# Optimization experiments

Hardware: AMD Instinct MI355X
Metric: run time of the kernel (lower is better)

Reference implementation:

```python
import jax, jax.numpy as jnp
import numpy as np

B, D, C = 8192, 64, 2048
BETA = 0.25
EPS = 1e-6


def setup_inputs() -> dict:
    key = jax.random.key(0)
    k1, k2, k3 = jax.random.split(key, 3)
    x = jax.random.normal(k1, (B, D), dtype=jnp.float32)
    prev_q = jax.random.normal(k2, (B, D), dtype=jnp.float32)
    codes = jax.random.normal(k3, (1, C, D), dtype=jnp.float32) * 0.1  # learned codebook param
    return {"x": x, "prev_q": prev_q, "codes": codes}


def _rotation_matrix(u, v, eps=EPS):
    # u: (B, D) unit vectors, v: (D,) unit vector. Rodrigues-like rotation mapping v -> u.
    uvT = u[:, :, None] * v[None, None, :]          # (B, D, D)
    vuT = v[None, :, None] * u[:, None, :]          # (B, D, D)
    A = uvT - vuT
    A2 = jnp.einsum('bij,bjk->bik', A, A)
    dot = jnp.sum(u * v[None, :], axis=-1)[:, None, None]  # (B,1,1)
    I = jnp.eye(u.shape[-1], dtype=u.dtype)
    return I[None] + A + A2 / (1.0 + dot + eps)


def reference(x, prev_q, codes):
    # F.normalize(prev_q, dim=-1, eps=1e-6)
    norm = jnp.linalg.norm(prev_q, axis=-1, keepdims=True)
    u = prev_q / jnp.maximum(norm, EPS)
    v = jnp.full((D,), 1.0 / float(D) ** 0.5, dtype=x.dtype)  # registered buffer v

    R = _rotation_matrix(u, v)                      # (B, D, D); R_inv = R^T
    x_canonical = jnp.einsum('bij,bi->bj', R, x)    # R^T @ x

    c0 = codes[0]                                   # (C, D)
    # squared L2 distances (B, C) via GEMM expansion (same math as sum((x-c)^2))
    dists = (jnp.sum(x_canonical ** 2, axis=-1, keepdims=True)
             - 2.0 * (x_canonical @ c0.T)
             + jnp.sum(c0 ** 2, axis=-1)[None, :])
    indices = jnp.argmin(dists, axis=-1)            # (B,)
    quantized_canonical = c0[indices]               # (B, D)

    # STE: value equals quantized_canonical, gradient flows to x_canonical
    q_out = x_canonical + jax.lax.stop_gradient(quantized_canonical - x_canonical)
    quantized = jnp.einsum('bij,bj->bi', R, q_out)  # R @ q_out

    loss_commit = jnp.mean(jnp.sum((x - jax.lax.stop_gradient(quantized_canonical)) ** 2, axis=-1))
    loss_codebook = jnp.mean(jnp.sum((jax.lax.stop_gradient(x) - quantized_canonical) ** 2, axis=-1))
    loss = loss_commit + BETA * loss_codebook
    return quantized, indices, loss
```

## Files before the change

kernel.cpp:

```cpp
#include <hip/hip_runtime.h>
#include <math.h>

#define B_ROWS 8192
#define DIM 64
#define NCODES 2048
#define NSPLIT 16
#define CODES_PER_SPLIT (NCODES / NSPLIT)
#define TILES_PER_WAVE (CODES_PER_SPLIT / 16)
#define EPSF 1e-6f
#define BETA 0.25f
#define V_VAL 0.125f

typedef __attribute__((ext_vector_type(8))) short sh8;
typedef __attribute__((ext_vector_type(4))) float f32x4;

__device__ __forceinline__ float wave_sum64(float v) {
#pragma unroll
    for (int m = 32; m >= 1; m >>= 1) v += __shfl_xor(v, m, 64);
    return v;
}

__device__ __forceinline__ unsigned short f2bf(float f) {
    unsigned u = __float_as_uint(f);
    unsigned r = (u + 0x7fffu + ((u >> 16) & 1u)) >> 16;
    return (unsigned short)r;
}
__device__ __forceinline__ float bf2f(unsigned short h) {
    return __uint_as_float(((unsigned)h) << 16);
}

__device__ __forceinline__ void write_frag3(unsigned short* frag, int rc,
                                            int dim, float val) {
    unsigned short s0 = f2bf(val);
    float r = val - bf2f(s0);
    unsigned short s1 = f2bf(r);
    r -= bf2f(s1);
    unsigned short s2 = f2bf(r);
    int t = rc >> 4, m = rc & 15;
    int h = dim >> 5, q = (dim >> 3) & 3, j = dim & 7;
    int lanep = q * 16 + m;
    size_t base = ((size_t)(t * 3) * 2 + h) * 512 + (size_t)lanep * 8 + j;
    frag[base] = s0;
    frag[base + 2 * 512] = s1;
    frag[base + 4 * 512] = s2;
}

__global__ __launch_bounds__(256) void rq_prep(
        const float* __restrict__ x,
        const float* __restrict__ pq,
        const float* __restrict__ codes,
        float* __restrict__ cn,
        unsigned short* __restrict__ cfrag,
        unsigned short* __restrict__ xfrag,
        float* __restrict__ uo,
        float* __restrict__ duv,
        float* __restrict__ out_loss) {
    int tid = threadIdx.x;
    int lane = tid & 63;
    int w = tid >> 6;

    if (blockIdx.x < NCODES / 4) {
        int c = blockIdx.x * 4 + w;
        float cv = codes[(size_t)c * DIM + lane];
        float s = wave_sum64(cv * cv);
        if (lane == 0) cn[c] = s;
        write_frag3(cfrag, c, lane, cv);
        if (blockIdx.x == 0 && tid == 0) *out_loss = 0.0f;
    } else {
        int r = (blockIdx.x - NCODES / 4) * 4 + w;
        float xv = x[(size_t)r * DIM + lane];
        float qv = pq[(size_t)r * DIM + lane];
        float n2 = wave_sum64(qv * qv);
        float inv = 1.0f / fmaxf(sqrtf(n2), EPSF);
        float uv = qv * inv;
        float d = V_VAL * wave_sum64(uv);
        float a = wave_sum64(uv * xv);
        float b = V_VAL * wave_sum64(xv);
        float den = 1.0f + d + EPSF;
        float cu = -b + (d * b - a) / den;
        float cv = a - (b - d * a) / den;
        float xcv = xv + uv * cu + V_VAL * cv;
        uo[(size_t)r * DIM + lane] = uv;
        if (lane == 0) duv[r] = d;
        write_frag3(xfrag, r, lane, xcv);
    }
}

__global__ __launch_bounds__(256) void rq_dist_mfma(
        const unsigned short* __restrict__ xfrag,
        const unsigned short* __restrict__ cfrag,
        const float* __restrict__ cn,
        float* __restrict__ pd,
        int* __restrict__ pi) {
    int tid = threadIdx.x;
    int lane = tid & 63;
    int w = tid >> 6;
    int rb = blockIdx.x >> 4;
    int cs = blockIdx.x & (NSPLIT - 1);
    int r0 = rb * 128 + w * 32;
    int rt0 = r0 >> 4;

    const sh8* xf = (const sh8*)xfrag;
    const sh8* cf = (const sh8*)cfrag;

    sh8 afr[2][3][2];
#pragma unroll
    for (int rs = 0; rs < 2; ++rs)
#pragma unroll
        for (int s = 0; s < 3; ++s)
#pragma unroll
            for (int h = 0; h < 2; ++h)
                afr[rs][s][h] = xf[(size_t)(((rt0 + rs) * 3 + s) * 2 + h) * 64 + lane];

    float bv0[4], bv1[4];
    int bi0[4], bi1[4];
#pragma unroll
    for (int i = 0; i < 4; ++i) {
        bv0[i] = INFINITY; bv1[i] = INFINITY;
        bi0[i] = 0x7fffffff; bi1[i] = 0x7fffffff;
    }

    int cbase = cs * CODES_PER_SPLIT;
    for (int t = 0; t < TILES_PER_WAVE; ++t) {
        int c0 = cbase + t * 16;
        int ct = c0 >> 4;
        sh8 bfr[3][2];
#pragma unroll
        for (int s = 0; s < 3; ++s)
#pragma unroll
            for (int h = 0; h < 2; ++h)
                bfr[s][h] = cf[(size_t)((ct * 3 + s) * 2 + h) * 64 + lane];

        f32x4 acc0 = {0.f, 0.f, 0.f, 0.f};
        f32x4 acc1 = {0.f, 0.f, 0.f, 0.f};
#pragma unroll
        for (int h = 0; h < 2; ++h) {
            acc0 = __builtin_amdgcn_mfma_f32_16x16x32_bf16(afr[0][2][h], bfr[0][h], acc0, 0, 0, 0);
            acc0 = __builtin_amdgcn_mfma_f32_16x16x32_bf16(afr[0][1][h], bfr[1][h], acc0, 0, 0, 0);
            acc0 = __builtin_amdgcn_mfma_f32_16x16x32_bf16(afr[0][0][h], bfr[2][h], acc0, 0, 0, 0);
            acc0 = __builtin_amdgcn_mfma_f32_16x16x32_bf16(afr[0][1][h], bfr[0][h], acc0, 0, 0, 0);
            acc0 = __builtin_amdgcn_mfma_f32_16x16x32_bf16(afr[0][0][h], bfr[1][h], acc0, 0, 0, 0);
            acc0 = __builtin_amdgcn_mfma_f32_16x16x32_bf16(afr[0][0][h], bfr[0][h], acc0, 0, 0, 0);

            acc1 = __builtin_amdgcn_mfma_f32_16x16x32_bf16(afr[1][2][h], bfr[0][h], acc1, 0, 0, 0);
            acc1 = __builtin_amdgcn_mfma_f32_16x16x32_bf16(afr[1][1][h], bfr[1][h], acc1, 0, 0, 0);
            acc1 = __builtin_amdgcn_mfma_f32_16x16x32_bf16(afr[1][0][h], bfr[2][h], acc1, 0, 0, 0);
            acc1 = __builtin_amdgcn_mfma_f32_16x16x32_bf16(afr[1][1][h], bfr[0][h], acc1, 0, 0, 0);
            acc1 = __builtin_amdgcn_mfma_f32_16x16x32_bf16(afr[1][0][h], bfr[1][h], acc1, 0, 0, 0);
            acc1 = __builtin_amdgcn_mfma_f32_16x16x32_bf16(afr[1][0][h], bfr[0][h], acc1, 0, 0, 0);
        }

        float cnv = cn[c0 + (lane & 15)];
        int idxv = c0 + (lane & 15);
#pragma unroll
        for (int reg = 0; reg < 4; ++reg) {
            float s0 = fmaf(-2.0f, acc0[reg], cnv);
            if (s0 < bv0[reg]) { bv0[reg] = s0; bi0[reg] = idxv; }
            float s1 = fmaf(-2.0f, acc1[reg], cnv);
            if (s1 < bv1[reg]) { bv1[reg] = s1; bi1[reg] = idxv; }
        }
    }

#pragma unroll
    for (int rs = 0; rs < 2; ++rs) {
#pragma unroll
        for (int reg = 0; reg < 4; ++reg) {
            float v = rs ? bv1[reg] : bv0[reg];
            int ix = rs ? bi1[reg] : bi0[reg];
#pragma unroll
            for (int m = 1; m < 16; m <<= 1) {
                float ov = __shfl_xor(v, m, 64);
                int oi = __shfl_xor(ix, m, 64);
                if (ov < v || (ov == v && oi < ix)) { v = ov; ix = oi; }
            }
            int row = r0 + rs * 16 + (lane >> 4) * 4 + reg;
            if ((lane & 15) == reg) {
                pd[(size_t)row * NSPLIT + cs] = v;
                pi[(size_t)row * NSPLIT + cs] = ix;
            }
        }
    }
}

__global__ __launch_bounds__(512) void rq_epilogue(
        const float* __restrict__ x,
        const float* __restrict__ codes,
        const float* __restrict__ uo,
        const float* __restrict__ duv,
        const float* __restrict__ pd,
        const int* __restrict__ pi,
        float* __restrict__ out_q,
        float* __restrict__ out_idx,
        float* __restrict__ out_loss) {
    __shared__ float s_part[8];
    int tid = threadIdx.x;
    int lane = tid & 63;
    int w = tid >> 6;
    int row0 = blockIdx.x * 64 + w * 8;

    float lsum = 0.f;
#pragma unroll
    for (int i = 0; i < 8; ++i) {
        int row = row0 + i;
        float pv = INFINITY;
        int iv = 0x7fffffff;
        if (lane < NSPLIT) {
            pv = pd[(size_t)row * NSPLIT + lane];
            iv = pi[(size_t)row * NSPLIT + lane];
        }
#pragma unroll
        for (int m = 1; m < NSPLIT; m <<= 1) {
            float ov = __shfl_xor(pv, m, 64);
            int oi = __shfl_xor(iv, m, 64);
            if (ov < pv || (ov == pv && oi < iv)) { pv = ov; iv = oi; }
        }
        int idx = __shfl(iv, 0, 64);

        float qc = codes[(size_t)idx * DIM + lane];
        float uvv = uo[(size_t)row * DIM + lane];
        float xv = x[(size_t)row * DIM + lane];
        float dv = duv[row];

        float aq = wave_sum64(uvv * qc);
        float bq = V_VAL * wave_sum64(qc);
        float den = 1.0f + dv + EPSF;
        float cu = bq + (dv * bq - aq) / den;
        float cw = -aq - (bq - dv * aq) / den;
        out_q[(size_t)row * DIM + lane] = qc + uvv * cu + V_VAL * cw;

        float diff = xv - qc;
        lsum += diff * diff;
        if (lane == 0) out_idx[row] = (float)idx;
    }
    lsum = wave_sum64(lsum);
    if (lane == 0) s_part[w] = lsum;
    __syncthreads();
    if (tid == 0) {
        float t = 0.f;
#pragma unroll
        for (int i = 0; i < 8; ++i) t += s_part[i];
        atomicAdd(out_loss, t * (1.0f + BETA) * (1.0f / (float)B_ROWS));
    }
}

extern "C" void kernel_launch(void* const* d_in, const int* in_sizes, int n_in,
                              void* d_out, int out_size, void* d_ws, size_t ws_size,
                              hipStream_t stream) {
    const float* x     = (const float*)d_in[0];
    const float* pq    = (const float*)d_in[1];
    const float* codes = (const float*)d_in[2];

    float* out      = (float*)d_out;
    float* out_q    = out;
    float* out_idx  = out + (size_t)B_ROWS * DIM;
    float* out_loss = out_idx + B_ROWS;

    char* ws = (char*)d_ws;
    const size_t MB = 1024 * 1024;
    float* uo            = (float*)ws;
    float* duv           = (float*)(ws + 2 * MB);
    float* cn            = (float*)(ws + 2 * MB + 64 * 1024);
    unsigned short* xfrg = (unsigned short*)(ws + 3 * MB);
    unsigned short* cfrg = (unsigned short*)(ws + 6 * MB);
    float* pd            = (float*)(ws + 7 * MB);
    int*   pi            = (int*)(ws + 7 * MB + 512 * 1024);

    rq_prep<<<NCODES / 4 + B_ROWS / 4, 256, 0, stream>>>(
        x, pq, codes, cn, cfrg, xfrg, uo, duv, out_loss);
    rq_dist_mfma<<<(B_ROWS / 128) * NSPLIT, 256, 0, stream>>>(
        xfrg, cfrg, cn, pd, pi);
    rq_epilogue<<<B_ROWS / 64, 512, 0, stream>>>(
        x, codes, uo, duv, pd, pi, out_q, out_idx, out_loss);
}
```

Before: 97.04 us.

## Stage codebook fragments in shared memory and batch row-prep wave reductions

```diff
diff --git a/kernel.cpp b/kernel.cpp
--- a/kernel.cpp
+++ b/kernel.cpp
@@ -70,12 +70,19 @@
         int r = (blockIdx.x - NCODES / 4) * 4 + w;
         float xv = x[(size_t)r * DIM + lane];
         float qv = pq[(size_t)r * DIM + lane];
-        float n2 = wave_sum64(qv * qv);
-        float inv = 1.0f / fmaxf(sqrtf(n2), EPSF);
+        float sqq = qv * qv, sq = qv, sqx = qv * xv, sx = xv;
+#pragma unroll
+        for (int m = 32; m >= 1; m >>= 1) {
+            sqq += __shfl_xor(sqq, m, 64);
+            sq  += __shfl_xor(sq,  m, 64);
+            sqx += __shfl_xor(sqx, m, 64);
+            sx  += __shfl_xor(sx,  m, 64);
+        }
+        float inv = 1.0f / fmaxf(sqrtf(sqq), EPSF);
         float uv = qv * inv;
-        float d = V_VAL * wave_sum64(uv);
-        float a = wave_sum64(uv * xv);
-        float b = V_VAL * wave_sum64(xv);
+        float d = V_VAL * sq * inv;
+        float a = inv * sqx;
+        float b = V_VAL * sx;
         float den = 1.0f + d + EPSF;
         float cu = -b + (d * b - a) / den;
         float cv = a - (b - d * a) / den;
@@ -92,6 +99,8 @@
         const float* __restrict__ cn,
         float* __restrict__ pd,
         int* __restrict__ pi) {
+    __shared__ sh8 sB[24 * 64];
+
     int tid = threadIdx.x;
     int lane = tid & 63;
     int w = tid >> 6;
@@ -99,6 +108,7 @@
     int cs = blockIdx.x & (NSPLIT - 1);
     int r0 = rb * 128 + w * 32;
     int rt0 = r0 >> 4;
+    int ct0 = cs * TILES_PER_WAVE;
 
     const sh8* xf = (const sh8*)xfrag;
     const sh8* cf = (const sh8*)cfrag;
@@ -121,44 +131,58 @@
     }
 
     int cbase = cs * CODES_PER_SPLIT;
-    for (int t = 0; t < TILES_PER_WAVE; ++t) {
-        int c0 = cbase + t * 16;
-        int ct = c0 >> 4;
-        sh8 bfr[3][2];
-#pragma unroll
-        for (int s = 0; s < 3; ++s)
-#pragma unroll
-            for (int h = 0; h < 2; ++h)
-                bfr[s][h] = cf[(size_t)((ct * 3 + s) * 2 + h) * 64 + lane];
-
-        f32x4 acc0 = {0.f, 0.f, 0.f, 0.f};
-        f32x4 acc1 = {0.f, 0.f, 0.f, 0.f};
-#pragma unroll
-        for (int h = 0; h < 2; ++h) {
-            acc0 = __builtin_amdgcn_mfma_f32_16x16x32_bf16(afr[0][2][h], bfr[0][h], acc0, 0, 0, 0);
-            acc0 = __builtin_amdgcn_mfma_f32_16x16x32_bf16(afr[0][1][h], bfr[1][h], acc0, 0, 0, 0);
-            acc0 = __builtin_amdgcn_mfma_f32_16x16x32_bf16(afr[0][0][h], bfr[2][h], acc0, 0, 0, 0);
-            acc0 = __builtin_amdgcn_mfma_f32_16x16x32_bf16(afr[0][1][h], bfr[0][h], acc0, 0, 0, 0);
-            acc0 = __builtin_amdgcn_mfma_f32_16x16x32_bf16(afr[0][0][h], bfr[1][h], acc0, 0, 0, 0);
-            acc0 = __builtin_amdgcn_mfma_f32_16x16x32_bf16(afr[0][0][h], bfr[0][h], acc0, 0, 0, 0);
-
-            acc1 = __builtin_amdgcn_mfma_f32_16x16x32_bf16(afr[1][2][h], bfr[0][h], acc1, 0, 0, 0);
-            acc1 = __builtin_amdgcn_mfma_f32_16x16x32_bf16(afr[1][1][h], bfr[1][h], acc1, 0, 0, 0);
-            acc1 = __builtin_amdgcn_mfma_f32_16x16x32_bf16(afr[1][0][h], bfr[2][h], acc1, 0, 0, 0);
-            acc1 = __builtin_amdgcn_mfma_f32_16x16x32_bf16(afr[1][1][h], bfr[0][h], acc1, 0, 0, 0);
-            acc1 = __builtin_amdgcn_mfma_f32_16x16x32_bf16(afr[1][0][h], bfr[1][h], acc1, 0, 0, 0);
-            acc1 = __builtin_amdgcn_mfma_f32_16x16x32_bf16(afr[1][0][h], bfr[0][h], acc1, 0, 0, 0);
-        }
-
-        float cnv = cn[c0 + (lane & 15)];
-        int idxv = c0 + (lane & 15);
-#pragma unroll
-        for (int reg = 0; reg < 4; ++reg) {
-            float s0 = fmaf(-2.0f, acc0[reg], cnv);
-            if (s0 < bv0[reg]) { bv0[reg] = s0; bi0[reg] = idxv; }
-            float s1 = fmaf(-2.0f, acc1[reg], cnv);
-            if (s1 < bv1[reg]) { bv1[reg] = s1; bi1[reg] = idxv; }
-        }
+#pragma unroll
+    for (int ch = 0; ch < 2; ++ch) {
+        {
+            int tloc = w;
+#pragma unroll
+            for (int sh = 0; sh < 6; ++sh) {
+                int fid = ((ct0 + ch * 4 + tloc) * 3 + (sh >> 1)) * 2 + (sh & 1);
+                sB[(tloc * 6 + sh) * 64 + lane] = cf[(size_t)fid * 64 + lane];
+            }
+        }
+        __syncthreads();
+
+#pragma unroll
+        for (int tloc = 0; tloc < 4; ++tloc) {
+            int c0 = cbase + (ch * 4 + tloc) * 16;
+            sh8 bfr[3][2];
+#pragma unroll
+            for (int s = 0; s < 3; ++s)
+#pragma unroll
+                for (int h = 0; h < 2; ++h)
+                    bfr[s][h] = sB[(tloc * 6 + s * 2 + h) * 64 + lane];
+
+            f32x4 acc0 = {0.f, 0.f, 0.f, 0.f};
+            f32x4 acc1 = {0.f, 0.f, 0.f, 0.f};
+#pragma unroll
+            for (int h = 0; h < 2; ++h) {
+                acc0 = __builtin_amdgcn_mfma_f32_16x16x32_bf16(afr[0][2][h], bfr[0][h], acc0, 0, 0, 0);
+                acc0 = __builtin_amdgcn_mfma_f32_16x16x32_bf16(afr[0][1][h], bfr[1][h], acc0, 0, 0, 0);
+                acc0 = __builtin_amdgcn_mfma_f32_16x16x32_bf16(afr[0][0][h], bfr[2][h], acc0, 0, 0, 0);
+                acc0 = __builtin_amdgcn_mfma_f32_16x16x32_bf16(afr[0][1][h], bfr[0][h], acc0, 0, 0, 0);
+                acc0 = __builtin_amdgcn_mfma_f32_16x16x32_bf16(afr[0][0][h], bfr[1][h], acc0, 0, 0, 0);
+                acc0 = __builtin_amdgcn_mfma_f32_16x16x32_bf16(afr[0][0][h], bfr[0][h], acc0, 0, 0, 0);
+
+                acc1 = __builtin_amdgcn_mfma_f32_16x16x32_bf16(afr[1][2][h], bfr[0][h], acc1, 0, 0, 0);
+                acc1 = __builtin_amdgcn_mfma_f32_16x16x32_bf16(afr[1][1][h], bfr[1][h], acc1, 0, 0, 0);
+                acc1 = __builtin_amdgcn_mfma_f32_16x16x32_bf16(afr[1][0][h], bfr[2][h], acc1, 0, 0, 0);
+                acc1 = __builtin_amdgcn_mfma_f32_16x16x32_bf16(afr[1][1][h], bfr[0][h], acc1, 0, 0, 0);
+                acc1 = __builtin_amdgcn_mfma_f32_16x16x32_bf16(afr[1][0][h], bfr[1][h], acc1, 0, 0, 0);
+                acc1 = __builtin_amdgcn_mfma_f32_16x16x32_bf16(afr[1][0][h], bfr[0][h], acc1, 0, 0, 0);
+            }
+
+            float cnv = cn[c0 + (lane & 15)];
+            int idxv = c0 + (lane & 15);
+#pragma unroll
+            for (int reg = 0; reg < 4; ++reg) {
+                float s0 = fmaf(-2.0f, acc0[reg], cnv);
+                if (s0 < bv0[reg]) { bv0[reg] = s0; bi0[reg] = idxv; }
+                float s1 = fmaf(-2.0f, acc1[reg], cnv);
+                if (s1 < bv1[reg]) { bv1[reg] = s1; bi1[reg] = idxv; }
+            }
+        }
+        __syncthreads();
     }
 
 #pragma unroll
```

Result: no change. 96.71 us (-0.3%).

## Batch prep reductions and spread epilogue over more blocks with separate loss reduce

Applied to the files above, without the earlier changes.

```diff
diff --git a/kernel.cpp b/kernel.cpp
--- a/kernel.cpp
+++ b/kernel.cpp
@@ -70,12 +70,19 @@
         int r = (blockIdx.x - NCODES / 4) * 4 + w;
         float xv = x[(size_t)r * DIM + lane];
         float qv = pq[(size_t)r * DIM + lane];
-        float n2 = wave_sum64(qv * qv);
-        float inv = 1.0f / fmaxf(sqrtf(n2), EPSF);
+        float sqq = qv * qv, sq = qv, sqx = qv * xv, sx = xv;
+#pragma unroll
+        for (int m = 32; m >= 1; m >>= 1) {
+            sqq += __shfl_xor(sqq, m, 64);
+            sq  += __shfl_xor(sq,  m, 64);
+            sqx += __shfl_xor(sqx, m, 64);
+            sx  += __shfl_xor(sx,  m, 64);
+        }
+        float inv = 1.0f / fmaxf(sqrtf(sqq), EPSF);
         float uv = qv * inv;
-        float d = V_VAL * wave_sum64(uv);
-        float a = wave_sum64(uv * xv);
-        float b = V_VAL * wave_sum64(xv);
+        float d = V_VAL * sq * inv;
+        float a = inv * sqx;
+        float b = V_VAL * sx;
         float den = 1.0f + d + EPSF;
         float cu = -b + (d * b - a) / den;
         float cv = a - (b - d * a) / den;
@@ -182,7 +189,7 @@
     }
 }
 
-__global__ __launch_bounds__(512) void rq_epilogue(
+__global__ __launch_bounds__(256) void rq_epilogue(
         const float* __restrict__ x,
         const float* __restrict__ codes,
         const float* __restrict__ uo,
@@ -191,17 +198,16 @@
         const int* __restrict__ pi,
         float* __restrict__ out_q,
         float* __restrict__ out_idx,
-        float* __restrict__ out_loss) {
-    __shared__ float s_part[8];
+        float* __restrict__ lossp) {
     int tid = threadIdx.x;
     int lane = tid & 63;
     int w = tid >> 6;
-    int row0 = blockIdx.x * 64 + w * 8;
+    int gw = blockIdx.x * 4 + w;
 
     float lsum = 0.f;
 #pragma unroll
-    for (int i = 0; i < 8; ++i) {
-        int row = row0 + i;
+    for (int i = 0; i < 2; ++i) {
+        int row = gw * 2 + i;
         float pv = INFINITY;
         int iv = 0x7fffffff;
         if (lane < NSPLIT) {
@@ -233,13 +239,23 @@
         if (lane == 0) out_idx[row] = (float)idx;
     }
     lsum = wave_sum64(lsum);
-    if (lane == 0) s_part[w] = lsum;
+    if (lane == 0) lossp[gw] = lsum;
+}
+
+__global__ void rq_loss_reduce(const float* __restrict__ lossp,
+                               float* __restrict__ out_loss) {
+    __shared__ float part[16];
+    int tid = threadIdx.x;
+    float s = 0.f;
+#pragma unroll
+    for (int i = 0; i < 4096 / 1024; ++i) s += lossp[tid + i * 1024];
+    s = wave_sum64(s);
+    if ((tid & 63) == 0) part[tid >> 6] = s;
     __syncthreads();
-    if (tid == 0) {
-        float t = 0.f;
-#pragma unroll
-        for (int i = 0; i < 8; ++i) t += s_part[i];
-        atomicAdd(out_loss, t * (1.0f + BETA) * (1.0f / (float)B_ROWS));
+    if (tid < 64) {
+        float v = (tid < 16) ? part[tid] : 0.f;
+        v = wave_sum64(v);
+        if (tid == 0) *out_loss = v * (1.0f + BETA) * (1.0f / (float)B_ROWS);
     }
 }
 
@@ -260,6 +276,7 @@
     float* uo            = (float*)ws;
     float* duv           = (float*)(ws + 2 * MB);
     float* cn            = (float*)(ws + 2 * MB + 64 * 1024);
+    float* lossp         = (float*)(ws + 2 * MB + 128 * 1024);
     unsigned short* xfrg = (unsigned short*)(ws + 3 * MB);
     unsigned short* cfrg = (unsigned short*)(ws + 6 * MB);
     float* pd            = (float*)(ws + 7 * MB);
@@ -269,6 +286,7 @@
         x, pq, codes, cn, cfrg, xfrg, uo, duv, out_loss);
     rq_dist_mfma<<<(B_ROWS / 128) * NSPLIT, 256, 0, stream>>>(
         xfrg, cfrg, cn, pd, pi);
-    rq_epilogue<<<B_ROWS / 64, 512, 0, stream>>>(
-        x, codes, uo, duv, pd, pi, out_q, out_idx, out_loss);
-}
+    rq_epilogue<<<B_ROWS / 8, 256, 0, stream>>>(
+        x, codes, uo, duv, pd, pi, out_q, out_idx, lossp);
+    rq_loss_reduce<<<1, 1024, 0, stream>>>(lossp, out_loss);
+}
```

Result: faster. 93.16 us (-4.0%).
